# Optimization experiments

Measured on AMD Instinct MI355X. Metric: run time of the kernel, lower is better.

The kernel has to match this reference:

```python
import jax, jax.numpy as jnp
import numpy as np

N_QUBITS = 12
N_LAYERS = 3
N_PARAMS = N_QUBITS * 3 * N_LAYERS  # 108
BATCH = 8192
DIM = 1 << N_QUBITS  # 4096


def _rx(theta):
    c = jnp.cos(theta / 2).astype(jnp.complex64)
    s = jnp.sin(theta / 2).astype(jnp.complex64)
    return jnp.stack([jnp.stack([c, -1j * s]), jnp.stack([-1j * s, c])])


def _ry(theta):
    c = jnp.cos(theta / 2).astype(jnp.complex64)
    s = jnp.sin(theta / 2).astype(jnp.complex64)
    return jnp.stack([jnp.stack([c, -s]), jnp.stack([s, c])])


def _rz(theta):
    e = jnp.exp(-1j * theta.astype(jnp.complex64) / 2)
    z = jnp.zeros((), jnp.complex64)
    return jnp.stack([jnp.stack([e, z]), jnp.stack([z, jnp.conj(e)])])


def _apply_1q(state, q, U):
    # state: (B,) + (2,)*n ; apply 2x2 gate U on wire q (axis q+1)
    s = jnp.moveaxis(state, q + 1, -1)
    s = s @ U.T
    return jnp.moveaxis(s, -1, q + 1)


def _cnot(state, c, t):
    # control wire c, target wire t (axes offset by 1 for batch dim)
    ca, ta = c + 1, t + 1
    s0 = jax.lax.index_in_dim(state, 0, ca, keepdims=False)
    s1 = jax.lax.index_in_dim(state, 1, ca, keepdims=False)
    ta2 = ta - 1 if ta > ca else ta  # target axis shifts after removing control axis
    s1 = jnp.flip(s1, axis=ta2)  # X on target (size-2 axis)
    return jnp.stack([s0, s1], axis=ca)


def setup_inputs() -> dict:
    key = jax.random.key(0)
    k1, k2 = jax.random.split(key)
    x = jax.random.normal(k1, (BATCH, DIM), dtype=jnp.float32)
    params = jax.random.normal(k2, (N_PARAMS,), dtype=jnp.float32) * 0.1
    return {"x": x, "params": params}


def reference(x, params):
    n = N_QUBITS
    B = x.shape[0]
    # AmplitudeEmbedding with normalize=True
    norm = jnp.linalg.norm(x, axis=1, keepdims=True)
    state = (x / norm).astype(jnp.complex64).reshape((B,) + (2,) * n)
    idx = 0
    for _ in range(N_LAYERS):
        for q in range(n):
            state = _apply_1q(state, q, _rx(params[idx])); idx += 1
            state = _apply_1q(state, q, _ry(params[idx])); idx += 1
            state = _apply_1q(state, q, _rz(params[idx])); idx += 1
        for q in range(n):
            state = _cnot(state, q, (q + 1) % n)
    # <Z_q> = P(q=0) - P(q=1)
    p = state.real ** 2 + state.imag ** 2  # (B,) + (2,)*n, float32
    outs = []
    for q in range(n):
        axes = tuple(a for a in range(1, n + 1) if a != q + 1)
        marg = jnp.sum(p, axis=axes)  # (B, 2)
        outs.append(marg[:, 0] - marg[:, 1])
    return jnp.stack(outs, axis=1)  # (B, n_qubits)
```

## Files before the change

kernel.cpp:

```cpp
#include <hip/hip_runtime.h>
#include <math.h>

#define NQ 12
#define DIM 4096
#define NGATES 36
#define NROUND 9

typedef float f32x4 __attribute__((ext_vector_type(4)));
typedef __fp16 fp16x2 __attribute__((ext_vector_type(2)));
typedef __fp16 fp16x4 __attribute__((ext_vector_type(4)));
typedef __fp16 fp16x8 __attribute__((ext_vector_type(8)));

constexpr unsigned swz(unsigned x) { return x ^ (x >> 4); }

struct Round {
  unsigned s[4];
  unsigned l[4];
  unsigned cbsw8[16];
  unsigned dt[4];
};
struct PlanT {
  Round rd[NROUND];
  unsigned zsel[NQ];
};

constexpr PlanT make_plan() {
  PlanT P{};
  unsigned Mcol[NQ] = {}, Minv[NQ] = {};
  for (int i = 0; i < NQ; ++i) { Mcol[i] = 1u << i; Minv[i] = 1u << i; }
  unsigned gm[NGATES] = {}, gs[NGATES] = {};
  int g = 0;
  for (int L = 0; L < 3; ++L) {
    for (int q = 0; q < NQ; ++q) { int b = NQ - 1 - q; gm[g] = Mcol[b]; gs[g] = Minv[b]; ++g; }
    for (int q = 0; q < NQ; ++q) {
      int bc = NQ - 1 - q, bt = NQ - 1 - ((q + 1) % NQ);
      Mcol[bc] ^= Mcol[bt];
      Minv[bt] ^= Minv[bc];
    }
  }
  for (int r = 0; r < NROUND; ++r) {
    unsigned m[4], red[4];
    for (int k = 0; k < 4; ++k) { m[k] = gm[4*r+k]; red[k] = m[k]; P.rd[r].s[k] = gs[4*r+k]; }
    for (int a = 0; a < 4; ++a) {
      unsigned p = red[a] & (0u - red[a]);
      for (int b = a + 1; b < 4; ++b) if (red[b] & p) red[b] ^= red[a];
    }
    unsigned piv[4];
    for (int a = 0; a < 4; ++a) piv[a] = red[a] & (0u - red[a]);
    for (int a = 0; a < 4; ++a)
      for (int b = a + 1; b < 4; ++b)
        if (piv[a] > piv[b]) { unsigned tp = piv[a]; piv[a] = piv[b]; piv[b] = tp; }
    for (int a = 0; a < 4; ++a) P.rd[r].l[a] = piv[a] - 1u;
    for (int d = 0; d < 16; ++d) {
      unsigned c = 0;
      for (int k = 0; k < 4; ++k) if (d & (1 << k)) c ^= m[k];
      P.rd[r].cbsw8[d] = swz(c) << 3;
    }
    for (int tt = 0; tt < 4; ++tt) {
      unsigned c = (unsigned)tt << 4;
      unsigned j = c;
      j = ((j & ~P.rd[r].l[0]) << 1) | (j & P.rd[r].l[0]);
      j = ((j & ~P.rd[r].l[1]) << 1) | (j & P.rd[r].l[1]);
      j = ((j & ~P.rd[r].l[2]) << 1) | (j & P.rd[r].l[2]);
      j = ((j & ~P.rd[r].l[3]) << 1) | (j & P.rd[r].l[3]);
      unsigned d = swz(j) << 3;
      for (int k = 0; k < 4; ++k)
        if (__builtin_popcount(j & P.rd[r].s[k]) & 1) d ^= P.rd[r].cbsw8[1u << k];
      P.rd[r].dt[tt] = d;
    }
  }
  for (int q = 0; q < NQ; ++q) P.zsel[q] = Minv[NQ - 1 - q];
  return P;
}

constexpr PlanT PLAN = make_plan();

__global__ void qc_prep(const float* __restrict__ params, __fp16* __restrict__ amat) {
  int t = threadIdx.x;
  int r = t >> 4, s = t & 15;
  if (r >= NROUND) return;
  float U[4][8];
  for (int k = 0; k < 4; ++k) {
    int gg = r * 4 + k;
    float h1 = params[3*gg+0]*0.5f, hh2 = params[3*gg+1]*0.5f, h3 = params[3*gg+2]*0.5f;
    float c1 = cosf(h1), s1 = sinf(h1);
    float c2 = cosf(hh2), s2 = sinf(hh2);
    float c3 = cosf(h3), s3 = sinf(h3);
    float a00r =  c2*c1, a00i =  s2*s1;
    float a01r = -s2*c1, a01i = -c2*s1;
    float a10r =  s2*c1, a10i = -c2*s1;
    float a11r =  c2*c1, a11i = -s2*s1;
    U[k][0] = c3*a00r + s3*a00i;  U[k][1] = c3*a00i - s3*a00r;
    U[k][2] = c3*a01r + s3*a01i;  U[k][3] = c3*a01i - s3*a01r;
    U[k][4] = c3*a10r - s3*a10i;  U[k][5] = c3*a10i + s3*a10r;
    U[k][6] = c3*a11r - s3*a11i;  U[k][7] = c3*a11i + s3*a11r;
  }
  __fp16* b0 = amat + r*2048 + s*32;
  __fp16* b1 = b0 + 512;
  __fp16* b2 = b0 + 1024;
  __fp16* b3 = b0 + 1536;
  for (int j = 0; j < 16; ++j) {
    float pr = 1.f, pi = 0.f;
    for (int k = 0; k < 4; ++k) {
      int idx = ((((s >> k) & 1) * 2) + ((j >> k) & 1)) * 2;
      float gr = U[k][idx], gi = U[k][idx + 1];
      float npr = pr * gr - pi * gi;
      pi = pr * gi + pi * gr;
      pr = npr;
    }
    float v0_ =  pr; __fp16 e0 = (__fp16)v0_;
    float v1_ = -pi; __fp16 e1 = (__fp16)v1_;
    float v2_ =  pi; __fp16 e2 = (__fp16)v2_;
    float v3_ =  pr; __fp16 e3 = (__fp16)v3_;
    b0[2*j]   = e0;  b1[2*j]   = (__fp16)(v0_ - (float)e0);
    b0[2*j+1] = e1;  b1[2*j+1] = (__fp16)(v1_ - (float)e1);
    b2[2*j]   = e2;  b3[2*j]   = (__fp16)(v2_ - (float)e2);
    b2[2*j+1] = e3;  b3[2*j+1] = (__fp16)(v3_ - (float)e3);
  }
}

__global__ __launch_bounds__(256)
__attribute__((amdgpu_waves_per_eu(4, 5)))
void qc_main(const float* __restrict__ x, const __fp16* __restrict__ amat,
             float* __restrict__ out) {
  __shared__ float2 sst[DIM];
  char* sb = (char*)sst;
  const int t = threadIdx.x;
  const long row = blockIdx.x;

  const float4* x4 = (const float4*)(x + (size_t)row * DIM);
  float ssq = 0.f;
#pragma unroll
  for (int k = 0; k < 4; ++k) {
    float4 a = x4[t + 256*k];
    int j0 = 4*(t + 256*k);
    *(float2*)(sb + (swz((unsigned)j0)     << 3)) = make_float2(a.x, 0.f);
    *(float2*)(sb + (swz((unsigned)(j0+1)) << 3)) = make_float2(a.y, 0.f);
    *(float2*)(sb + (swz((unsigned)(j0+2)) << 3)) = make_float2(a.z, 0.f);
    *(float2*)(sb + (swz((unsigned)(j0+3)) << 3)) = make_float2(a.w, 0.f);
    ssq += a.x*a.x + a.y*a.y + a.z*a.z + a.w*a.w;
  }
#pragma unroll
  for (int off = 32; off > 0; off >>= 1) ssq += __shfl_down(ssq, off, 64);
  __syncthreads();

#pragma unroll 1
  for (int r = 0; r < NROUND; ++r) {
    const unsigned s0 = PLAN.rd[r].s[0], sA = PLAN.rd[r].s[1];
    const unsigned sB = PLAN.rd[r].s[2], sC = PLAN.rd[r].s[3];
    const unsigned l0 = PLAN.rd[r].l[0], l1 = PLAN.rd[r].l[1];
    const unsigned l2 = PLAN.rd[r].l[2], l3 = PLAN.rd[r].l[3];
    const unsigned CB1 = PLAN.rd[r].cbsw8[1], CB2 = PLAN.rd[r].cbsw8[2];
    const unsigned CB3 = PLAN.rd[r].cbsw8[3];
    const unsigned C4 = PLAN.rd[r].cbsw8[4], C8 = PLAN.rd[r].cbsw8[8];
    const unsigned D1 = PLAN.rd[r].dt[1], D2 = PLAN.rd[r].dt[2];
    const unsigned D3 = PLAN.rd[r].dt[3];

    unsigned j = ((unsigned)t & 0xC0u) | ((unsigned)t & 15u);
    j = ((j & ~l0) << 1) | (j & l0);
    j = ((j & ~l1) << 1) | (j & l1);
    j = ((j & ~l2) << 1) | (j & l2);
    j = ((j & ~l3) << 1) | (j & l3);
    unsigned adj8 = 0;
    adj8 ^= (unsigned)(-(int)(__popc(j & s0) & 1)) & CB1;
    adj8 ^= (unsigned)(-(int)(__popc(j & sA) & 1)) & CB2;
    adj8 ^= (unsigned)(-(int)(__popc(j & sB) & 1)) & C4;
    adj8 ^= (unsigned)(-(int)(__popc(j & sC) & 1)) & C8;
    const unsigned q = ((unsigned)t >> 4) & 3u;
    const unsigned qsel = ((q & 1u) ? C4 : 0u) ^ ((q & 2u) ? C8 : 0u);
    const unsigned b0a = (((j ^ (j >> 4)) << 3) ^ adj8) ^ qsel;

    const fp16x8* am = (const fp16x8*)(amat + (size_t)r * 2048);
    const int fo = (t & 15) * 4 + (int)q;
    const fp16x8 Arh = am[fo];
    const fp16x8 Arl = am[64 + fo];
    const fp16x8 Aih = am[128 + fo];
    const fp16x8 Ail = am[192 + fo];

#pragma unroll
    for (int tt = 0; tt < 4; ++tt) {
      const unsigned bb = b0a ^ (tt == 0 ? 0u : tt == 1 ? D1 : tt == 2 ? D2 : D3);
      const unsigned a0 = bb, a1 = bb ^ CB1, a2 = bb ^ CB2, a3 = bb ^ CB3;
      const float2 A0 = *(const float2*)(sb + a0);
      const float2 A1 = *(const float2*)(sb + a1);
      const float2 A2 = *(const float2*)(sb + a2);
      const float2 A3 = *(const float2*)(sb + a3);
      fp16x2 p0 = __builtin_amdgcn_cvt_pkrtz(A0.x, A0.y);
      fp16x2 p1 = __builtin_amdgcn_cvt_pkrtz(A1.x, A1.y);
      fp16x2 p2 = __builtin_amdgcn_cvt_pkrtz(A2.x, A2.y);
      fp16x2 p3 = __builtin_amdgcn_cvt_pkrtz(A3.x, A3.y);
      fp16x2 q0 = __builtin_amdgcn_cvt_pkrtz(A0.x - (float)p0[0], A0.y - (float)p0[1]);
      fp16x2 q1 = __builtin_amdgcn_cvt_pkrtz(A1.x - (float)p1[0], A1.y - (float)p1[1]);
      fp16x2 q2 = __builtin_amdgcn_cvt_pkrtz(A2.x - (float)p2[0], A2.y - (float)p2[1]);
      fp16x2 q3 = __builtin_amdgcn_cvt_pkrtz(A3.x - (float)p3[0], A3.y - (float)p3[1]);
      fp16x4 u01 = __builtin_shufflevector(p0, p1, 0, 1, 2, 3);
      fp16x4 u23 = __builtin_shufflevector(p2, p3, 0, 1, 2, 3);
      fp16x8 Bhi = __builtin_shufflevector(u01, u23, 0, 1, 2, 3, 4, 5, 6, 7);
      fp16x4 w01 = __builtin_shufflevector(q0, q1, 0, 1, 2, 3);
      fp16x4 w23 = __builtin_shufflevector(q2, q3, 0, 1, 2, 3);
      fp16x8 Blo = __builtin_shufflevector(w01, w23, 0, 1, 2, 3, 4, 5, 6, 7);

      f32x4 are = {0.f, 0.f, 0.f, 0.f}, aim = {0.f, 0.f, 0.f, 0.f};
      are = __builtin_amdgcn_mfma_f32_16x16x32_f16(Arh, Bhi, are, 0, 0, 0);
      are = __builtin_amdgcn_mfma_f32_16x16x32_f16(Arl, Bhi, are, 0, 0, 0);
      are = __builtin_amdgcn_mfma_f32_16x16x32_f16(Arh, Blo, are, 0, 0, 0);
      aim = __builtin_amdgcn_mfma_f32_16x16x32_f16(Aih, Bhi, aim, 0, 0, 0);
      aim = __builtin_amdgcn_mfma_f32_16x16x32_f16(Ail, Bhi, aim, 0, 0, 0);
      aim = __builtin_amdgcn_mfma_f32_16x16x32_f16(Aih, Blo, aim, 0, 0, 0);

      *(float2*)(sb + a0) = make_float2(are[0], aim[0]);
      *(float2*)(sb + a1) = make_float2(are[1], aim[1]);
      *(float2*)(sb + a2) = make_float2(are[2], aim[2]);
      *(float2*)(sb + a3) = make_float2(are[3], aim[3]);
    }
    __syncthreads();
  }

  const unsigned mbase8 = (((16u * (unsigned)t) ^ (unsigned)t) << 3);
  float p[16];
#pragma unroll
  for (int c = 0; c < 16; ++c) {
    float2 v = *(const float2*)(sb + (mbase8 ^ ((unsigned)c << 3)));
    p[c] = v.x * v.x + v.y * v.y;
  }
#pragma unroll
  for (int b = 0; b < 4; ++b) {
#pragma unroll
    for (int c = 0; c < 16; ++c) {
      if (!(c & (1 << b))) {
        const int c1 = c | (1 << b);
        float u = p[c], v = p[c1];
        p[c] = u + v; p[c1] = u - v;
      }
    }
  }
  float zs[NQ];
#pragma unroll
  for (int qq = 0; qq < NQ; ++qq) {
    const unsigned m = PLAN.zsel[qq];
    const float v = p[m & 15u];
    const int sgn = __popc((unsigned)t & (m >> 4)) & 1;
    zs[qq] = sgn ? -v : v;
  }

  __syncthreads();
#pragma unroll
  for (int k = 0; k < 6; ++k)
    *(float2*)(sb + (((unsigned)(k << 8) + (unsigned)t) << 3)) =
        make_float2(zs[2*k], zs[2*k+1]);
  if ((t & 63) == 0) *(float*)(sb + 12288 + (t >> 6) * 4) = ssq;
  __syncthreads();
  if (t < 192) {
    const int k = t >> 5, j = t & 31;
    const char* cbp = sb + (k << 11) + (j << 3);
    float2 acc = *(const float2*)(cbp);
#pragma unroll
    for (int i = 1; i < 8; ++i) {
      float2 vv = *(const float2*)(cbp + i * 256);
      acc.x += vv.x; acc.y += vv.y;
    }
#pragma unroll
    for (int off = 16; off > 0; off >>= 1) {
      acc.x += __shfl_down(acc.x, off, 32);
      acc.y += __shfl_down(acc.y, off, 32);
    }
    if (j == 0) *(float2*)(sb + 12352 + (k << 3)) = acc;
  }
  __syncthreads();
  if (t < NQ) {
    const float* sq = (const float*)(sb + 12288);
    const float den = sq[0] + sq[1] + sq[2] + sq[3];
    out[row * NQ + t] = ((const float*)(sb + 12352))[t] / den;
  }
}

extern "C" void kernel_launch(void* const* d_in, const int* in_sizes, int n_in,
                              void* d_out, int out_size, void* d_ws, size_t ws_size,
                              hipStream_t stream) {
  const float* x = (const float*)d_in[0];
  const float* params = (const float*)d_in[1];
  float* out = (float*)d_out;
  __fp16* amat = (__fp16*)d_ws;
  const int nrows = in_sizes[0] / DIM;
  qc_prep<<<dim3(1), dim3(256), 0, stream>>>(params, amat);
  qc_main<<<dim3(nrows), dim3(256), 0, stream>>>(x, amat, out);
}
```

Before: 302.3 us.

## Search per-round gate order and thread-bit mapping to avoid LDS bank conflicts

The compile-time plan now searches, for each round, over gate permutations and over which four of the eight free index bits map to the lane-column thread bits. It picks a choice whose resulting LDS addresses span all bank groups (a rank-4 check), then builds the thread index as an XOR of per-bit offsets instead of bit insertion. The prep kernel reorders the gate matrices to match. The goal is to cut LDS bank conflicts in the gathered shared-memory loads of each round, at the cost of a more complex constexpr plan and a fallback when no mapping qualifies.

```diff
diff --git a/kernel.cpp b/kernel.cpp
--- a/kernel.cpp
+++ b/kernel.cpp
@@ -12,10 +12,27 @@
 typedef __fp16 fp16x8 __attribute__((ext_vector_type(8)));
 
 constexpr unsigned swz(unsigned x) { return x ^ (x >> 4); }
+constexpr int pc(unsigned x) { int c = 0; while (x) { c += (int)(x & 1u); x >>= 1; } return c; }
+
+constexpr bool rank4(const unsigned* v, int n) {
+  unsigned pivs[4] = {0, 0, 0, 0};
+  int rk = 0;
+  for (int i = 0; i < n; ++i) {
+    unsigned x = v[i] & 15u;
+    for (int bit = 3; bit >= 0; --bit) {
+      if (!((x >> bit) & 1u)) continue;
+      if (pivs[bit]) x ^= pivs[bit];
+      else { pivs[bit] = x; ++rk; break; }
+    }
+  }
+  return rk == 4;
+}
 
 struct Round {
   unsigned s[4];
-  unsigned l[4];
+  unsigned gidx[4];
+  unsigned colD[4];
+  unsigned waveD[2];
   unsigned cbsw8[16];
   unsigned dt[4];
 };
@@ -39,34 +56,82 @@
     }
   }
   for (int r = 0; r < NROUND; ++r) {
-    unsigned m[4], red[4];
-    for (int k = 0; k < 4; ++k) { m[k] = gm[4*r+k]; red[k] = m[k]; P.rd[r].s[k] = gs[4*r+k]; }
+    unsigned m0[4], sl0[4];
+    for (int k = 0; k < 4; ++k) { m0[k] = gm[4*r+k]; sl0[k] = gs[4*r+k]; }
+    unsigned red[4];
+    for (int k = 0; k < 4; ++k) red[k] = m0[k];
     for (int a = 0; a < 4; ++a) {
-      unsigned p = red[a] & (0u - red[a]);
-      for (int b = a + 1; b < 4; ++b) if (red[b] & p) red[b] ^= red[a];
+      unsigned pp = red[a] & (0u - red[a]);
+      for (int b = a + 1; b < 4; ++b) if (red[b] & pp) red[b] ^= red[a];
     }
     unsigned piv[4];
     for (int a = 0; a < 4; ++a) piv[a] = red[a] & (0u - red[a]);
     for (int a = 0; a < 4; ++a)
       for (int b = a + 1; b < 4; ++b)
         if (piv[a] > piv[b]) { unsigned tp = piv[a]; piv[a] = piv[b]; piv[b] = tp; }
-    for (int a = 0; a < 4; ++a) P.rd[r].l[a] = piv[a] - 1u;
+    unsigned l[4];
+    for (int a = 0; a < 4; ++a) l[a] = piv[a] - 1u;
+    unsigned D[8];
+    for (int i = 0; i < 8; ++i) {
+      unsigned j = 1u << i;
+      j = ((j & ~l[0]) << 1) | (j & l[0]);
+      j = ((j & ~l[1]) << 1) | (j & l[1]);
+      j = ((j & ~l[2]) << 1) | (j & l[2]);
+      j = ((j & ~l[3]) << 1) | (j & l[3]);
+      D[i] = j;
+    }
+    const int gp[3][4] = {{0,1,2,3},{0,2,1,3},{0,3,1,2}};
+    int bp = -1; unsigned bS = 0;
+    for (int p = 0; p < 3 && bp < 0; ++p) {
+      unsigned mm[4], ss[4];
+      for (int k = 0; k < 4; ++k) { mm[k] = m0[gp[p][k]]; ss[k] = sl0[gp[p][k]]; }
+      unsigned cbu[16];
+      for (int d = 0; d < 16; ++d) {
+        unsigned c = 0;
+        for (int k = 0; k < 4; ++k) if ((d >> k) & 1) c ^= mm[k];
+        cbu[d] = swz(c);
+      }
+      for (unsigned S = 0; S < 256 && bp < 0; ++S) {
+        if (pc(S) != 4) continue;
+        unsigned v[6]; int vi = 0;
+        for (int i = 0; i < 8; ++i) if ((S >> i) & 1) {
+          unsigned av = swz(D[i]);
+          for (int k = 0; k < 4; ++k) if (pc(D[i] & ss[k]) & 1) av ^= cbu[1u << k];
+          v[vi++] = av;
+        }
+        v[4] = cbu[4]; v[5] = cbu[8];
+        if (rank4(v, 6)) { bp = p; bS = S; }
+      }
+    }
+    if (bp < 0) { bp = 0; bS = 0x0Fu; }
+    unsigned mm[4];
+    for (int k = 0; k < 4; ++k) {
+      P.rd[r].gidx[k] = (unsigned)gp[bp][k];
+      P.rd[r].s[k]    = sl0[gp[bp][k]];
+      mm[k]           = m0[gp[bp][k]];
+    }
+    unsigned cbu[16];
     for (int d = 0; d < 16; ++d) {
       unsigned c = 0;
-      for (int k = 0; k < 4; ++k) if (d & (1 << k)) c ^= m[k];
-      P.rd[r].cbsw8[d] = swz(c) << 3;
-    }
+      for (int k = 0; k < 4; ++k) if ((d >> k) & 1) c ^= mm[k];
+      cbu[d] = swz(c);
+      P.rd[r].cbsw8[d] = cbu[d] << 3;
+    }
+    unsigned cD[4], TD[2], WD[2];
+    int nc = 0, other[4]; int no = 0;
+    for (int i = 0; i < 8; ++i) {
+      if ((bS >> i) & 1) cD[nc++] = D[i];
+      else other[no++] = i;
+    }
+    TD[0] = D[other[0]]; TD[1] = D[other[1]];
+    WD[0] = D[other[2]]; WD[1] = D[other[3]];
+    for (int k = 0; k < 4; ++k) P.rd[r].colD[k] = cD[k];
+    P.rd[r].waveD[0] = WD[0]; P.rd[r].waveD[1] = WD[1];
     for (int tt = 0; tt < 4; ++tt) {
-      unsigned c = (unsigned)tt << 4;
-      unsigned j = c;
-      j = ((j & ~P.rd[r].l[0]) << 1) | (j & P.rd[r].l[0]);
-      j = ((j & ~P.rd[r].l[1]) << 1) | (j & P.rd[r].l[1]);
-      j = ((j & ~P.rd[r].l[2]) << 1) | (j & P.rd[r].l[2]);
-      j = ((j & ~P.rd[r].l[3]) << 1) | (j & P.rd[r].l[3]);
-      unsigned d = swz(j) << 3;
-      for (int k = 0; k < 4; ++k)
-        if (__builtin_popcount(j & P.rd[r].s[k]) & 1) d ^= P.rd[r].cbsw8[1u << k];
-      P.rd[r].dt[tt] = d;
+      unsigned jt = ((tt & 1) ? TD[0] : 0u) ^ ((tt & 2) ? TD[1] : 0u);
+      unsigned d8 = swz(jt);
+      for (int k = 0; k < 4; ++k) if (pc(jt & P.rd[r].s[k]) & 1) d8 ^= cbu[1u << k];
+      P.rd[r].dt[tt] = d8 << 3;
     }
   }
   for (int q = 0; q < NQ; ++q) P.zsel[q] = Minv[NQ - 1 - q];
@@ -81,7 +146,7 @@
   if (r >= NROUND) return;
   float U[4][8];
   for (int k = 0; k < 4; ++k) {
-    int gg = r * 4 + k;
+    int gg = r * 4 + (int)PLAN.rd[r].gidx[k];
     float h1 = params[3*gg+0]*0.5f, hh2 = params[3*gg+1]*0.5f, h3 = params[3*gg+2]*0.5f;
     float c1 = cosf(h1), s1 = sinf(h1);
     float c2 = cosf(hh2), s2 = sinf(hh2);
@@ -148,19 +213,21 @@
   for (int r = 0; r < NROUND; ++r) {
     const unsigned s0 = PLAN.rd[r].s[0], sA = PLAN.rd[r].s[1];
     const unsigned sB = PLAN.rd[r].s[2], sC = PLAN.rd[r].s[3];
-    const unsigned l0 = PLAN.rd[r].l[0], l1 = PLAN.rd[r].l[1];
-    const unsigned l2 = PLAN.rd[r].l[2], l3 = PLAN.rd[r].l[3];
+    const unsigned cD0 = PLAN.rd[r].colD[0], cD1 = PLAN.rd[r].colD[1];
+    const unsigned cD2 = PLAN.rd[r].colD[2], cD3 = PLAN.rd[r].colD[3];
+    const unsigned W0 = PLAN.rd[r].waveD[0], W1 = PLAN.rd[r].waveD[1];
     const unsigned CB1 = PLAN.rd[r].cbsw8[1], CB2 = PLAN.rd[r].cbsw8[2];
     const unsigned CB3 = PLAN.rd[r].cbsw8[3];
     const unsigned C4 = PLAN.rd[r].cbsw8[4], C8 = PLAN.rd[r].cbsw8[8];
-    const unsigned D1 = PLAN.rd[r].dt[1], D2 = PLAN.rd[r].dt[2];
-    const unsigned D3 = PLAN.rd[r].dt[3];
-
-    unsigned j = ((unsigned)t & 0xC0u) | ((unsigned)t & 15u);
-    j = ((j & ~l0) << 1) | (j & l0);
-    j = ((j & ~l1) << 1) | (j & l1);
-    j = ((j & ~l2) << 1) | (j & l2);
-    j = ((j & ~l3) << 1) | (j & l3);
+    const unsigned dts[4] = {0u, PLAN.rd[r].dt[1], PLAN.rd[r].dt[2], PLAN.rd[r].dt[3]};
+
+    unsigned j = 0;
+    j ^= (unsigned)(-(int)((t >> 0) & 1)) & cD0;
+    j ^= (unsigned)(-(int)((t >> 1) & 1)) & cD1;
+    j ^= (unsigned)(-(int)((t >> 2) & 1)) & cD2;
+    j ^= (unsigned)(-(int)((t >> 3) & 1)) & cD3;
+    j ^= (unsigned)(-(int)((t >> 6) & 1)) & W0;
+    j ^= (unsigned)(-(int)((t >> 7) & 1)) & W1;
     unsigned adj8 = 0;
     adj8 ^= (unsigned)(-(int)(__popc(j & s0) & 1)) & CB1;
     adj8 ^= (unsigned)(-(int)(__popc(j & sA) & 1)) & CB2;
@@ -179,7 +246,7 @@
 
 #pragma unroll
     for (int tt = 0; tt < 4; ++tt) {
-      const unsigned bb = b0a ^ (tt == 0 ? 0u : tt == 1 ? D1 : tt == 2 ? D2 : D3);
+      const unsigned bb = b0a ^ dts[tt];
       const unsigned a0 = bb, a1 = bb ^ CB1, a2 = bb ^ CB2, a3 = bb ^ CB3;
       const float2 A0 = *(const float2*)(sb + a0);
       const float2 A1 = *(const float2*)(sb + a1);
```

New measurement: 305.0 us. Within noise of the previous version (+0.9%).
